# Kernel optimization log

Hardware: AMD Instinct MI355X
Metric: run time of the kernel (lower is better)

The kernel has to match this reference:

```python
import jax, jax.numpy as jnp
import numpy as np

GROUPS = 8   # GroupNorm groups used by create_pat_conv*_blocks(..., groups=8)
EPS = 1e-5
K = 20       # num_neighbor


def group_norm(x, gamma, beta):
    # x: [B, C, ...spatial]
    B, C = x.shape[0], x.shape[1]
    shape = x.shape
    xg = x.reshape(B, GROUPS, C // GROUPS, -1)
    m = xg.mean(axis=(2, 3), keepdims=True)
    v = ((xg - m) ** 2).mean(axis=(2, 3), keepdims=True)
    xg = (xg - m) * jax.lax.rsqrt(v + EPS)
    x = xg.reshape(shape)
    bshape = (1, C) + (1,) * (len(shape) - 2)
    return x * gamma.reshape(bshape) + beta.reshape(bshape)


def conv_block(x, w, b, gamma, beta):
    # pointwise (kernel-size 1) conv + GroupNorm + ELU, works for 1d and 2d spatial
    y = jnp.einsum('oc,bc...->bo...', w, x) + b.reshape((1, -1) + (1,) * (x.ndim - 2))
    return jax.nn.elu(group_norm(y, gamma, beta))


def knn_graph(points, k):
    # points: [B, 3, N] -> neighbor coords [B, 3, N, k] (self included, dilation=1)
    sq = jnp.sum(points * points, axis=1)                      # [B, N]
    inner = jnp.einsum('bci,bcj->bij', points, points)         # [B, N, N]
    dist = sq[:, :, None] + sq[:, None, :] - 2.0 * inner       # squared pairwise dist
    _, idx = jax.lax.top_k(-dist, k)                           # [B, N, k] smallest dists
    neighbors = jnp.take_along_axis(points[:, :, None, :], idx[:, None, :, :], axis=3)
    return neighbors                                           # [B, 3, N, k]


def setup_inputs() -> dict:
    key = jax.random.key(0)
    B, N = 4, 8192
    dims1 = [6, 32, 64]
    dims2 = [64, 512, 1024]
    keys = iter(jax.random.split(key, 32))
    inp = {"points": jax.random.normal(next(keys), (B, 3, N), dtype=jnp.float32)}
    for tag, dims in (("p1", dims1), ("p2", dims2)):
        for i in range(len(dims) - 1):
            cin, cout = dims[i], dims[i + 1]
            inp[f"{tag}_w{i}"] = jax.random.normal(next(keys), (cout, cin), dtype=jnp.float32) / np.float32(np.sqrt(cin))
            inp[f"{tag}_b{i}"] = jnp.zeros((cout,), dtype=jnp.float32)
            inp[f"{tag}_g{i}"] = jnp.ones((cout,), dtype=jnp.float32)
            inp[f"{tag}_beta{i}"] = jnp.zeros((cout,), dtype=jnp.float32)
    return inp


def reference(points, p1_w0, p1_b0, p1_g0, p1_beta0, p1_w1, p1_b1, p1_g1, p1_beta1,
              p2_w0, p2_b0, p2_g0, p2_beta0, p2_w1, p2_b1, p2_g1, p2_beta1):
    neighbors = knn_graph(points, K)                             # [B, 3, N, K]
    center = jnp.broadcast_to(points[:, :, :, None], neighbors.shape)
    x = jnp.concatenate([center, neighbors - center], axis=1)   # [B, 6, N, K]
    x = conv_block(x, p1_w0, p1_b0, p1_g0, p1_beta0)            # [B, 32, N, K]
    x = conv_block(x, p1_w1, p1_b1, p1_g1, p1_beta1)            # [B, 64, N, K]
    x = jnp.max(x, axis=2)                                      # [B, 64, K] (faithful to source: max over dim=2)
    x = conv_block(x, p2_w0, p2_b0, p2_g0, p2_beta0)            # [B, 512, K]
    x = conv_block(x, p2_w1, p2_b1, p2_g1, p2_beta1)            # [B, 1024, K]
    return x
```

## Files before the change

kernel.cpp:

```cpp
#include <hip/hip_runtime.h>
#include <math.h>

#define NPTS   8192
#define BATCH  4
#define KNN    20
#define NKTOT  (NPTS*KNN)
#define EPS    1e-5f
#define FQC    64

#define WINW   3072
#define WITR   (WINW/4/128)
#define GWIN   2048
#define GITR   (GWIN/4/128)
#define NBIN   1024
#define BIN_LO (-4.5f)
#define BIN_W  (9.0f/1024.0f)

typedef float v2f __attribute__((ext_vector_type(2)));

__device__ __forceinline__ float elu(float x) { return x > 0.0f ? x : expm1f(x); }
__device__ __forceinline__ float eluf(float x) { return x > 0.0f ? x : __expf(x) - 1.0f; }
__device__ __forceinline__ v2f splat2(float x) { v2f v; v.x = x; v.y = x; return v; }
__device__ __forceinline__ float rfl(float x) {
    return __uint_as_float(__builtin_amdgcn_readfirstlane(__float_as_uint(x)));
}

__device__ __forceinline__ unsigned fenc(float f) {
    unsigned b = __float_as_uint(f);
    return b ^ ((unsigned)(((int)b) >> 31) | 0x80000000u);
}
__device__ __forceinline__ float fdec(unsigned u) {
    unsigned b = (u & 0x80000000u) ? (u ^ 0x80000000u) : ~u;
    return __uint_as_float(b);
}

__device__ __forceinline__ int xbin(float x) {
    int bin = (int)floorf((x + 4.5f) * (1024.0f / 9.0f));
    return bin < 0 ? 0 : (bin > NBIN - 1 ? NBIN - 1 : bin);
}

__device__ __forceinline__ unsigned long long packkey(float s, int orig, int slot) {
    return ((unsigned long long)fenc(s) << 32)
         | (unsigned)(((NPTS - 1 - orig) << 13) | slot);
}

__global__ __launch_bounds__(256) void prep_kernel(const float* __restrict__ points,
                                                   float4* __restrict__ pts4,
                                                   float* __restrict__ zeroreg,
                                                   unsigned* __restrict__ minenc,
                                                   unsigned* __restrict__ fcnt,
                                                   int* __restrict__ Pcur_part)
{
    __shared__ int lh[NBIN];
    const int t = blockIdx.x * 256 + threadIdx.x;
    const int b = t >> 13, n = t & (NPTS - 1);
    for (int i = threadIdx.x; i < NBIN; i += 256) lh[i] = 0;
    const float* px = points + b * 3 * NPTS;
    float x = px[n], y = px[NPTS + n], z = px[2 * NPTS + n];
    pts4[t] = make_float4(x, y, z, -0.5f * (x * x + y * y + z * z));
    if (t < 18176) zeroreg[t] = 0.f;
    if (t < 5120)  minenc[t] = 0xFFFFFFFFu;
    if (t < 8)     fcnt[t] = 0u;
    __syncthreads();
    atomicAdd(&lh[xbin(x)], 1);
    __syncthreads();
    for (int i = threadIdx.x; i < NBIN; i += 256)
        Pcur_part[blockIdx.x * NBIN + i] = lh[i];
}

__global__ __launch_bounds__(256) void scatter_kernel(const float4* __restrict__ pts4,
                                                      const int* __restrict__ Pcur_part,
                                                      float4* __restrict__ psort,
                                                      int* __restrict__ sidx,
                                                      int* __restrict__ binof)
{
    __shared__ int boff[NBIN];
    __shared__ int brank[NBIN];
    __shared__ int wsum[256];
    const int jb = blockIdx.x & 31;
    const int b  = blockIdx.x >> 5;
    const int tt = threadIdx.x;
    const int t0 = tt * 4;

    int tot0 = 0, tot1 = 0, tot2 = 0, tot3 = 0;
    int pre0 = 0, pre1 = 0, pre2 = 0, pre3 = 0;
    for (int p = 0; p < 32; ++p) {
        const int4 c = *(const int4*)&Pcur_part[(b * 32 + p) * NBIN + t0];
        tot0 += c.x; tot1 += c.y; tot2 += c.z; tot3 += c.w;
        if (p < jb) { pre0 += c.x; pre1 += c.y; pre2 += c.z; pre3 += c.w; }
    }
    const int tsum = tot0 + tot1 + tot2 + tot3;
    wsum[tt] = tsum;
    __syncthreads();
    for (int off = 1; off < 256; off <<= 1) {
        int a = (tt >= off) ? wsum[tt - off] : 0;
        __syncthreads();
        wsum[tt] += a;
        __syncthreads();
    }
    int run = wsum[tt] - tsum;
    boff[t0 + 0] = run + pre0; run += tot0;
    boff[t0 + 1] = run + pre1; run += tot1;
    boff[t0 + 2] = run + pre2; run += tot2;
    boff[t0 + 3] = run + pre3;
    for (int i = tt; i < NBIN; i += 256) brank[i] = 0;
    __syncthreads();

    const int n = jb * 256 + tt;
    float4 p = pts4[b * NPTS + n];
    int bin = xbin(p.x);
    int slot = boff[bin] + atomicAdd(&brank[bin], 1);
    psort[b * NPTS + slot] = p;
    sidx [b * NPTS + slot] = n;
    binof[b * NPTS + slot] = bin;
}

__global__ __launch_bounds__(256, 8) void knn_win_kernel(
    const float4* __restrict__ psort, const int* __restrict__ sidx,
    const int* __restrict__ binof, int* __restrict__ idx_out,
    unsigned* __restrict__ fcnt, int* __restrict__ flist)
{
    __shared__ unsigned long long queue[8][FQC];
    __shared__ float smaxs[4][8][64];
    __shared__ float gates[8];
    __shared__ int qcnt[8];

    const int tid  = threadIdx.x;
    const int lane = tid & 63;
    const int wv   = tid >> 6;
    const int b    = blockIdx.x >> 10;
    const int oct  = blockIdx.x & 1023;
    const int q0s  = oct * 8;
    const float4* psb = psort + b * NPTS;
    const int*    six = sidx  + b * NPTS;
    const int*    bob = binof + b * NPTS;

    int s = q0s + 4 - WINW / 2;
    if (s < 0) s = 0;
    if (s > NPTS - WINW) s = NPTS - WINW;
    int gs = q0s + 4 - GWIN / 2;
    if (gs < 0) gs = 0;
    if (gs > NPTS - GWIN) gs = NPTS - GWIN;

    if (tid < 8) qcnt[tid] = 0;

    float qx[8], qy[8], qz[8], q2[8];
    v2f smax2[8];
#pragma unroll
    for (int q = 0; q < 8; ++q) {
        float4 qp = psb[q0s + q];
        qx[q] = rfl(qp.x); qy[q] = rfl(qp.y); qz[q] = rfl(qp.z);
        q2[q] = rfl(-(qp.w + qp.w));
        smax2[q] = splat2(-INFINITY);
    }

    const int gbase = gs + (((lane >> 5) * 4 + wv) << 6) + ((lane & 31) << 1);
    const int lbase = s  + (((lane >> 5) * 4 + wv) << 6) + ((lane & 31) << 1);

#pragma unroll
    for (int t = 0; t < GITR; ++t) {
        float4 p0 = psb[gbase + t * 512];
        float4 p1 = psb[gbase + t * 512 + 1];
        v2f px = { p0.x, p1.x }, py = { p0.y, p1.y };
        v2f pz = { p0.z, p1.z }, pw = { p0.w, p1.w };
#pragma unroll
        for (int q = 0; q < 8; ++q) {
            v2f sv = __builtin_elementwise_fma(splat2(qx[q]), px,
                     __builtin_elementwise_fma(splat2(qy[q]), py,
                     __builtin_elementwise_fma(splat2(qz[q]), pz, pw)));
            smax2[q] = __builtin_elementwise_max(smax2[q], sv);
        }
    }
#pragma unroll
    for (int q = 0; q < 8; ++q) smaxs[wv][q][lane] = fmaxf(smax2[q].x, smax2[q].y);
    __syncthreads();

#pragma unroll
    for (int qq = 0; qq < 2; ++qq) {
        const int q = wv * 2 + qq;
        float v = fmaxf(fmaxf(smaxs[0][q][lane], smaxs[1][q][lane]),
                        fmaxf(smaxs[2][q][lane], smaxs[3][q][lane]));
#pragma unroll
        for (int k = 2; k <= 64; k <<= 1)
#pragma unroll
            for (int j = k >> 1; j >= 1; j >>= 1) {
                float o = __shfl_xor(v, j);
                bool up = ((lane & k) == 0);
                bool keepmin = (((lane & j) == 0) == up);
                v = keepmin ? fminf(v, o) : fmaxf(v, o);
            }
        float m = __shfl(v, 44);
        if (lane == 0) gates[q] = m - 1e-4f - 1e-5f * fabsf(m);
    }
    __syncthreads();
    float sgate[8];
#pragma unroll
    for (int q = 0; q < 8; ++q) sgate[q] = gates[q];

#pragma unroll
    for (int t = 0; t < WITR; ++t) {
        const int jb = lbase + t * 512;
        float4 p0 = psb[jb];
        float4 p1 = psb[jb + 1];
        v2f px = { p0.x, p1.x }, py = { p0.y, p1.y };
        v2f pz = { p0.z, p1.z }, pw = { p0.w, p1.w };
#pragma unroll
        for (int q = 0; q < 8; ++q) {
            v2f sv = __builtin_elementwise_fma(splat2(qx[q]), px,
                     __builtin_elementwise_fma(splat2(qy[q]), py,
                     __builtin_elementwise_fma(splat2(qz[q]), pz, pw)));
            if (fmaxf(sv.x, sv.y) >= sgate[q]) {
#pragma unroll
                for (int h = 0; h < 2; ++h) {
                    float svh = h ? sv.y : sv.x;
                    if (svh >= sgate[q]) {
                        int slot = atomicAdd(&qcnt[q], 1);
                        if (slot < FQC)
                            queue[q][slot] = packkey(svh, six[jb + h], jb + h);
                    }
                }
            }
        }
    }
    __syncthreads();

    float xLe = (s == 0) ? -3.0e38f
                         : (BIN_LO + (float)(bob[s] + 1) * BIN_W);
    float xRe = (s == NPTS - WINW) ? 3.0e38f
                         : (BIN_LO + (float)bob[s + WINW] * BIN_W);

#pragma unroll
    for (int qq = 0; qq < 2; ++qq) {
        const int q = wv * 2 + qq;
        const int cr = qcnt[q];
        const bool ovf = (cr > FQC);
        const int c = cr < FQC ? cr : FQC;
        unsigned long long key = (lane < c) ? queue[q][lane] : 0ull;
#pragma unroll
        for (int k = 2; k <= 64; k <<= 1)
#pragma unroll
            for (int j = k >> 1; j >= 1; j >>= 1) {
                unsigned long long o = __shfl_xor(key, j);
                bool up = ((lane & k) == 0);
                bool keepmax = (((lane & j) == 0) == up);
                bool omax = o > key;
                key = (keepmax == omax) ? o : key;
            }
        if (lane < KNN)
            idx_out[(b * KNN + lane) * NPTS + (q0s + q)] =
                (int)(unsigned)(key & 0x1FFFu);

        unsigned long long k19 = __shfl(key, 19);
        float s20 = fdec((unsigned)(k19 >> 32));
        float d20 = fmaxf(q2[q] - 2.0f * s20, 0.0f);
        float mg  = 1e-3f + 1e-3f * d20;
        float dL  = qx[q] - xLe;
        float dR  = xRe - qx[q];
        bool ok = !ovf && (c >= KNN) && dL > 0.0f && dR > 0.0f
                  && (d20 + mg < dL * dL) && (d20 + mg < dR * dR);
        if (!ok && lane == 0) {
            unsigned fs = atomicAdd(&fcnt[b], 1u);
            if (fs < 8192u) flist[b * 8192 + fs] = q0s + q;
        }
    }
}

__global__ __launch_bounds__(256, 8) void knn_fb_kernel(const float4* __restrict__ psort,
                                                        const int* __restrict__ sidx,
                                                        int* __restrict__ idx_out,
                                                        const unsigned* __restrict__ fcnt,
                                                        const int* __restrict__ flist)
{
    __shared__ unsigned long long queue[2][FQC];
    __shared__ float smaxs[4][2][64];
    __shared__ float gates[2];
    __shared__ int qcnt[2];

    const int tid  = threadIdx.x;
    const int lane = tid & 63;
    const int wv   = tid >> 6;
    const int bb   = blockIdx.x & 3;
    unsigned cnt = fcnt[bb];
    if (cnt > 8192u) cnt = 8192u;
    if (cnt == 0u) return;
    const float4* pb = psort + bb * NPTS;
    const int* six = sidx + bb * NPTS;
    const int* fl = flist + bb * 8192;
    const int cbase = wv * (NPTS / 4);
    const int tstep = gridDim.x >> 2;

    for (int task = blockIdx.x >> 2; task * 2 < (int)cnt; task += tstep) {
        int qs[2];
        float qx[2], qy[2], qz[2];
        v2f smax2[2];
        if (tid < 2) qcnt[tid] = 0;
#pragma unroll
        for (int q = 0; q < 2; ++q) {
            int e = task * 2 + q;
            if (e >= (int)cnt) e = (int)cnt - 1;
            qs[q] = __builtin_amdgcn_readfirstlane(fl[e]);
            float4 qp = pb[qs[q]];
            qx[q] = rfl(qp.x); qy[q] = rfl(qp.y); qz[q] = rfl(qp.z);
            smax2[q] = splat2(-INFINITY);
        }

#pragma unroll 4
        for (int t = 0; t < NPTS / 4 / 128; ++t) {
            float4 p0 = pb[cbase + t * 128 + 2 * lane];
            float4 p1 = pb[cbase + t * 128 + 2 * lane + 1];
            v2f px = { p0.x, p1.x }, py = { p0.y, p1.y };
            v2f pz = { p0.z, p1.z }, pw = { p0.w, p1.w };
#pragma unroll
            for (int q = 0; q < 2; ++q) {
                v2f sv = __builtin_elementwise_fma(splat2(qx[q]), px,
                         __builtin_elementwise_fma(splat2(qy[q]), py,
                         __builtin_elementwise_fma(splat2(qz[q]), pz, pw)));
                smax2[q] = __builtin_elementwise_max(smax2[q], sv);
            }
        }
#pragma unroll
        for (int q = 0; q < 2; ++q) smaxs[wv][q][lane] = fmaxf(smax2[q].x, smax2[q].y);
        __syncthreads();

        if (wv < 2) {
            const int q = wv;
            float v = fmaxf(fmaxf(smaxs[0][q][lane], smaxs[1][q][lane]),
                            fmaxf(smaxs[2][q][lane], smaxs[3][q][lane]));
#pragma unroll
            for (int k = 2; k <= 64; k <<= 1)
#pragma unroll
                for (int j = k >> 1; j >= 1; j >>= 1) {
                    float o = __shfl_xor(v, j);
                    bool up = ((lane & k) == 0);
                    bool keepmin = (((lane & j) == 0) == up);
                    v = keepmin ? fminf(v, o) : fmaxf(v, o);
                }
            float m = __shfl(v, 44);
            if (lane == 0) gates[q] = m - 1e-4f - 1e-5f * fabsf(m);
        }
        __syncthreads();
        float sg0 = gates[0], sg1 = gates[1];

        for (int t = 0; t < NPTS / 4 / 128; ++t) {
            const int jb = cbase + t * 128 + 2 * lane;
            float4 p0 = pb[jb];
            float4 p1 = pb[jb + 1];
            v2f px = { p0.x, p1.x }, py = { p0.y, p1.y };
            v2f pz = { p0.z, p1.z }, pw = { p0.w, p1.w };
#pragma unroll
            for (int q = 0; q < 2; ++q) {
                float sg = q ? sg1 : sg0;
                v2f sv = __builtin_elementwise_fma(splat2(qx[q]), px,
                         __builtin_elementwise_fma(splat2(qy[q]), py,
                         __builtin_elementwise_fma(splat2(qz[q]), pz, pw)));
                if (fmaxf(sv.x, sv.y) >= sg) {
#pragma unroll
                    for (int h = 0; h < 2; ++h) {
                        float svh = h ? sv.y : sv.x;
                        if (svh >= sg) {
                            int slot = atomicAdd(&qcnt[q], 1);
                            if (slot < FQC)
                                queue[q][slot] = packkey(svh, six[jb + h], jb + h);
                        }
                    }
                }
            }
        }
        __syncthreads();

        if (wv < 2) {
            const int q = wv;
            int c = qcnt[q]; c = c < FQC ? c : FQC;
            unsigned long long key = (lane < c) ? queue[q][lane] : 0ull;
#pragma unroll
            for (int k = 2; k <= 64; k <<= 1)
#pragma unroll
                for (int j = k >> 1; j >= 1; j >>= 1) {
                    unsigned long long o = __shfl_xor(key, j);
                    bool up = ((lane & k) == 0);
                    bool keepmax = (((lane & j) == 0) == up);
                    bool omax = o > key;
                    key = (keepmax == omax) ? o : key;
                }
            if (lane < KNN)
                idx_out[(bb * KNN + lane) * NPTS + qs[q]] =
                    (int)(unsigned)(key & 0x1FFFu);
        }
        __syncthreads();
    }
}

__global__ __launch_bounds__(256) void moments_x_kernel(const float4* __restrict__ psort,
                                                        const int* __restrict__ idx,
                                                        float* __restrict__ sums1p)
{
    const int b  = blockIdx.x / 80;
    const int r0 = (blockIdx.x - b * 80) * 2048;
    const float4* pb = psort + b * NPTS;
    const int* ib = idx + b * NKTOT;

    float v[27];
#pragma unroll
    for (int i = 0; i < 27; ++i) v[i] = 0.f;

    for (int e = 0; e < 8; ++e) {
        const int id = r0 + e * 256 + threadIdx.x;
        const int n = id & (NPTS - 1);
        const int j = ib[id];
        float4 c4 = pb[n];
        float4 e4 = pb[j];
        float x[6] = { c4.x, c4.y, c4.z, e4.x - c4.x, e4.y - c4.y, e4.z - c4.z };
        int p = 6;
#pragma unroll
        for (int d = 0; d < 6; ++d) {
            v[d] += x[d];
#pragma unroll
            for (int ee = d; ee < 6; ++ee) v[p++] += x[d] * x[ee];
        }
    }
#pragma unroll
    for (int i = 0; i < 27; ++i)
        for (int o = 32; o > 0; o >>= 1) v[i] += __shfl_xor(v[i], o);

    __shared__ float red[4][27];
    const int lane = threadIdx.x & 63, w = threadIdx.x >> 6;
    if (lane == 0)
#pragma unroll
        for (int i = 0; i < 27; ++i) red[w][i] = v[i];
    __syncthreads();
    if (threadIdx.x < 27) {
        float acc = red[0][threadIdx.x] + red[1][threadIdx.x] + red[2][threadIdx.x] + red[3][threadIdx.x];
        int slot = blockIdx.x & 63;
        atomicAdd(&sums1p[(slot * BATCH + b) * 27 + threadIdx.x], acc);
    }
}

__global__ void finalize1_kernel(const float* __restrict__ sums1p,
                                 const float* __restrict__ w1, const float* __restrict__ b1,
                                 const float* __restrict__ g1, const float* __restrict__ beta1,
                                 float* __restrict__ w1f)
{
    __shared__ float S[BATCH][27];
    const int t = threadIdx.x;
    if (t < 108) {
        int b = t / 27, i = t % 27;
        float acc = 0.f;
        for (int s = 0; s < 64; ++s) acc += sums1p[(s * BATCH + b) * 27 + i];
        S[b][i] = acc;
    }
    __syncthreads();
    const int b = t >> 5, c = t & 31;
    const float invS = 1.0f / (float)NKTOT;
    float Ex[6], M[6][6];
#pragma unroll
    for (int d = 0; d < 6; ++d) Ex[d] = S[b][d] * invS;
    int p = 6;
#pragma unroll
    for (int d = 0; d < 6; ++d)
#pragma unroll
        for (int e = d; e < 6; ++e) { float v = S[b][p++] * invS; M[d][e] = v; M[e][d] = v; }
    const int g = c >> 2;
    float msum = 0.f, qsum = 0.f;
    for (int cc = g * 4; cc < g * 4 + 4; ++cc) {
        float w[6];
#pragma unroll
        for (int d = 0; d < 6; ++d) w[d] = w1[cc * 6 + d];
        float dotEx = 0.f;
#pragma unroll
        for (int d = 0; d < 6; ++d) dotEx += w[d] * Ex[d];
        float Ey = dotEx + b1[cc];
        float Ey2 = 0.f;
#pragma unroll
        for (int d = 0; d < 6; ++d)
#pragma unroll
            for (int e = 0; e < 6; ++e) Ey2 += w[d] * w[e] * M[d][e];
        Ey2 += 2.0f * b1[cc] * dotEx + b1[cc] * b1[cc];
        msum += Ey; qsum += Ey2;
    }
    float m = msum * 0.25f;
    float var = qsum * 0.25f - m * m;
    float inv = rsqrtf(var + EPS);
    float s = g1[c] * inv;
    float tt = s * (b1[c] - m) + beta1[c];
    float* o = w1f + (b * 32 + c) * 8;
#pragma unroll
    for (int d = 0; d < 6; ++d) o[d] = s * w1[c * 6 + d];
    o[6] = tt; o[7] = 0.f;
}

__global__ __launch_bounds__(256, 3) void fused_main_kernel(
    const float4* __restrict__ psort, const int* __restrict__ idxb,
    const float* __restrict__ w1f, const float* __restrict__ w2, const float* __restrict__ b2,
    float* __restrict__ sums2p, unsigned int* __restrict__ maxenc, unsigned int* __restrict__ minenc)
{
    __shared__ __align__(16) float w2t[32 * 64];
    __shared__ __align__(16) float z1s[32 * 256];
    __shared__ __align__(16) float4 w1s4[64];
    __shared__ float b2s[64];
    __shared__ float redmx[256], redmn[256], sqred[64];

    const int t   = threadIdx.x;
    const int blk = blockIdx.x;
    const int nc  = blk & 15;
    const int k   = (blk >> 4) % 20;
    const int b   = blk / 320;

    for (int i = t; i < 512; i += 256) {
        float4 v = ((const float4*)w2)[i];
        int c = i >> 3, kq = (i & 7) * 4;
        w2t[(kq + 0) * 64 + c] = v.x; w2t[(kq + 1) * 64 + c] = v.y;
        w2t[(kq + 2) * 64 + c] = v.z; w2t[(kq + 3) * 64 + c] = v.w;
    }
    if (t < 64) { w1s4[t] = ((const float4*)w1f)[b * 64 + t]; b2s[t] = b2[t]; }

    const int wvi = t >> 6;
    const int cg8 = t & 7;
    const int n0  = (t >> 3) * 8;
    const int c0  = cg8 * 8;
    const float4* pb = psort + b * NPTS;
    const int nbase = nc * 512;
    const int* idxrow = idxb + (b * KNN + k) * NPTS;

    float mx[8], mn[8];
#pragma unroll
    for (int ci = 0; ci < 8; ++ci) { mx[ci] = -INFINITY; mn[ci] = INFINITY; }
    float gs = 0.f, gq = 0.f;

    for (int ph = 0; ph < 2; ++ph) {
        const int n = nbase + ph * 256 + t;
        const int j = idxrow[n];
        float4 c4 = pb[n];
        float4 e4 = pb[j];
        float x0[6] = { c4.x, c4.y, c4.z, e4.x - c4.x, e4.y - c4.y, e4.z - c4.z };

        __syncthreads();
#pragma unroll
        for (int c = 0; c < 32; ++c) {
            float4 wA = w1s4[c * 2 + 0];
            float4 wB = w1s4[c * 2 + 1];
            float z = wB.z;
            z = fmaf(wA.x, x0[0], z); z = fmaf(wA.y, x0[1], z); z = fmaf(wA.z, x0[2], z);
            z = fmaf(wA.w, x0[3], z); z = fmaf(wB.x, x0[4], z); z = fmaf(wB.y, x0[5], z);
            z1s[c * 256 + t] = eluf(z);
        }
        __syncthreads();

        float acc[8][8];
#pragma unroll
        for (int ci = 0; ci < 8; ++ci) {
            float bb = b2s[c0 + ci];
#pragma unroll
            for (int pj = 0; pj < 8; ++pj) acc[ci][pj] = bb;
        }
#pragma unroll
        for (int kk = 0; kk < 32; ++kk) {
            float4 a0 = *(const float4*)&w2t[kk * 64 + c0];
            float4 a1 = *(const float4*)&w2t[kk * 64 + c0 + 4];
            float4 z0 = *(const float4*)&z1s[kk * 256 + n0];
            float4 z1v = *(const float4*)&z1s[kk * 256 + n0 + 4];
            float avv[8] = { a0.x, a0.y, a0.z, a0.w, a1.x, a1.y, a1.z, a1.w };
            float zvv[8] = { z0.x, z0.y, z0.z, z0.w, z1v.x, z1v.y, z1v.z, z1v.w };
#pragma unroll
            for (int ci = 0; ci < 8; ++ci)
#pragma unroll
                for (int pj = 0; pj < 8; ++pj) acc[ci][pj] = fmaf(avv[ci], zvv[pj], acc[ci][pj]);
        }
#pragma unroll
        for (int ci = 0; ci < 8; ++ci)
#pragma unroll
            for (int pj = 0; pj < 8; ++pj) {
                float v = acc[ci][pj];
                gs += v; gq = fmaf(v, v, gq);
                mx[ci] = fmaxf(mx[ci], v); mn[ci] = fminf(mn[ci], v);
            }
    }

#pragma unroll
    for (int m = 8; m <= 32; m <<= 1) {
#pragma unroll
        for (int ci = 0; ci < 8; ++ci) {
            mx[ci] = fmaxf(mx[ci], __shfl_xor(mx[ci], m));
            mn[ci] = fminf(mn[ci], __shfl_xor(mn[ci], m));
        }
        gs += __shfl_xor(gs, m);
        gq += __shfl_xor(gq, m);
    }
    if ((t & 63) < 8) {
        const int l = t & 7;
#pragma unroll
        for (int ci = 0; ci < 8; ++ci) {
            redmx[wvi * 64 + l * 8 + ci] = mx[ci];
            redmn[wvi * 64 + l * 8 + ci] = mn[ci];
        }
        sqred[(wvi * 8 + l) * 2 + 0] = gs;
        sqred[(wvi * 8 + l) * 2 + 1] = gq;
    }
    __syncthreads();
    if (t < 64) {
        float m = fmaxf(fmaxf(redmx[t], redmx[64 + t]), fmaxf(redmx[128 + t], redmx[192 + t]));
        atomicMax(&maxenc[(b * 64 + t) * KNN + k], fenc(m));
    } else if (t < 128) {
        int c = t - 64;
        float m = fminf(fminf(redmn[c], redmn[64 + c]), fminf(redmn[128 + c], redmn[192 + c]));
        atomicMin(&minenc[(b * 64 + c) * KNN + k], fenc(m));
    } else if (t < 144) {
        int i2 = t - 128, g = i2 >> 1, w = i2 & 1;
        float v = 0.f;
#pragma unroll
        for (int wv2 = 0; wv2 < 4; ++wv2)
            v += sqred[(wv2 * 8 + g) * 2 + w];
        int slot = blk & 63;
        atomicAdd(&sums2p[((slot * BATCH + b) * 8 + g) * 2 + w], v);
    }
}

__global__ void build_m1_kernel(const float* __restrict__ sums2p,
                                const unsigned int* __restrict__ maxenc,
                                const unsigned int* __restrict__ minenc,
                                const float* __restrict__ gamma, const float* __restrict__ beta,
                                float* __restrict__ m1)
{
    const int t = blockIdx.x * 256 + threadIdx.x;
    const int b = t / 1280;
    const int r = t - b * 1280;
    const int c = r / 20;
    const int g = c >> 3;
    float s = 0.f, q = 0.f;
    for (int sl = 0; sl < 64; ++sl) {
        s += sums2p[((sl * BATCH + b) * 8 + g) * 2 + 0];
        q += sums2p[((sl * BATCH + b) * 8 + g) * 2 + 1];
    }
    const float cnt = 8.0f * (float)NKTOT;
    float m = s / cnt;
    float var = q / cnt - m * m;
    float inv = rsqrtf(var + EPS);
    float sc = gamma[c] * inv;
    float tt = beta[c] - sc * m;
    float y = (sc >= 0.f) ? fdec(maxenc[t]) : fdec(minenc[t]);
    m1[t] = elu(sc * y + tt);
}

template <int CIN, int SLOTS>
__global__ void p2_gemm_kernel(const float* __restrict__ zin, const float* __restrict__ w,
                               const float* __restrict__ bias, float* __restrict__ yout,
                               float* __restrict__ sumsp, int chans_per_group)
{
    const int t = blockIdx.x * 256 + threadIdx.x;
    const int per_b = (gridDim.x * 256) / BATCH;
    const int b = t / per_b;
    const int r = t - b * per_b;
    const int o = r / 20;
    const int k = r - o * 20;
    const float* zb = zin + b * CIN * 20;
    const float* wrow = w + o * CIN;
    float acc = bias[o];
    for (int c = 0; c < CIN; c += 4) {
        float4 wv = *(const float4*)&wrow[c];
        acc += wv.x * zb[(c + 0) * 20 + k] + wv.y * zb[(c + 1) * 20 + k]
             + wv.z * zb[(c + 2) * 20 + k] + wv.w * zb[(c + 3) * 20 + k];
    }
    yout[t] = acc;

    __shared__ float ls[16];
    if (threadIdx.x < 16) ls[threadIdx.x] = 0.f;
    __syncthreads();
    const int g = o / chans_per_group;
    atomicAdd(&ls[g * 2 + 0], acc);
    atomicAdd(&ls[g * 2 + 1], acc * acc);
    __syncthreads();
    if (threadIdx.x < 16) {
        int slot = blockIdx.x & (SLOTS - 1);
        atomicAdd(&sumsp[(slot * BATCH + b) * 16 + threadIdx.x], ls[threadIdx.x]);
    }
}

template <int SLOTS>
__global__ void p2_finalize_kernel(const float* __restrict__ y, const float* __restrict__ sumsp,
                                   const float* __restrict__ gamma, const float* __restrict__ beta,
                                   float* __restrict__ z, int chans_per_group, float cnt)
{
    const int t = blockIdx.x * 256 + threadIdx.x;
    const int per_b = (gridDim.x * 256) / BATCH;
    const int b = t / per_b;
    const int r = t - b * per_b;
    const int o = r / 20;
    const int g = o / chans_per_group;
    float s = 0.f, q = 0.f;
    for (int sl = 0; sl < SLOTS; ++sl) {
        s += sumsp[(sl * BATCH + b) * 16 + g * 2 + 0];
        q += sumsp[(sl * BATCH + b) * 16 + g * 2 + 1];
    }
    float m = s / cnt;
    float var = q / cnt - m * m;
    float inv = rsqrtf(var + EPS);
    float v = gamma[o] * inv * (y[t] - m) + beta[o];
    z[t] = elu(v);
}

extern "C" void kernel_launch(void* const* d_in, const int* in_sizes, int n_in,
                              void* d_out, int out_size, void* d_ws, size_t ws_size,
                              hipStream_t stream)
{
    const float* points  = (const float*)d_in[0];
    const float* p1_w0   = (const float*)d_in[1];
    const float* p1_b0   = (const float*)d_in[2];
    const float* p1_g0   = (const float*)d_in[3];
    const float* p1_bt0  = (const float*)d_in[4];
    const float* p1_w1   = (const float*)d_in[5];
    const float* p1_b1   = (const float*)d_in[6];
    const float* p1_g1   = (const float*)d_in[7];
    const float* p1_bt1  = (const float*)d_in[8];
    const float* p2_w0   = (const float*)d_in[9];
    const float* p2_b0   = (const float*)d_in[10];
    const float* p2_g0   = (const float*)d_in[11];
    const float* p2_bt0  = (const float*)d_in[12];
    const float* p2_w1   = (const float*)d_in[13];
    const float* p2_b1   = (const float*)d_in[14];
    const float* p2_g1   = (const float*)d_in[15];
    const float* p2_bt1  = (const float*)d_in[16];
    float* out = (float*)d_out;

    float* ws = (float*)d_ws;
    int*      idx     = (int*)ws;
    float*    sums1p  = ws + 655360;
    float*    sums2p  = sums1p + 6912;
    float*    sumsAp  = sums2p + 4096;
    float*    sumsBp  = sumsAp + 1024;
    unsigned* maxenc  = (unsigned*)(sumsBp + 1024);
    unsigned* minenc  = maxenc + 5120;
    float*    w1f     = (float*)(minenc + 5120);
    float*    m1      = w1f + 1024;
    float*    yp2a    = m1 + 5120;
    float*    zp2a    = yp2a + 40960;
    float*    yp2b    = zp2a + 40960;
    float4*   pts4    = (float4*)yp2a;
    int*      Pcur_part = idx;
    float*    psortf  = yp2b + 81920;
    float4*   psort4  = (float4*)psortf;
    int*      sidx    = (int*)(psortf + 131072);
    int*      binof   = sidx + 32768;
    unsigned* fcnt8   = (unsigned*)(binof + 32768 + 64);
    int*      flist   = (int*)(fcnt8 + 64);

    prep_kernel<<<128, 256, 0, stream>>>(points, pts4, sums1p, minenc, fcnt8, Pcur_part);
    scatter_kernel<<<128, 256, 0, stream>>>(pts4, Pcur_part, psort4, sidx, binof);
    knn_win_kernel<<<4096, 256, 0, stream>>>(psort4, sidx, binof, idx, fcnt8, flist);
    knn_fb_kernel<<<4096, 256, 0, stream>>>(psort4, sidx, idx, fcnt8, flist);
    moments_x_kernel<<<320, 256, 0, stream>>>(psort4, idx, sums1p);
    finalize1_kernel<<<1, 128, 0, stream>>>(sums1p, p1_w0, p1_b0, p1_g0, p1_bt0, w1f);
    fused_main_kernel<<<1280, 256, 0, stream>>>(psort4, idx, w1f, p1_w1, p1_b1,
                                                sums2p, maxenc, minenc);
    build_m1_kernel<<<20, 256, 0, stream>>>(sums2p, maxenc, minenc, p1_g1, p1_bt1, m1);
    p2_gemm_kernel<64, 16><<<160, 256, 0, stream>>>(m1, p2_w0, p2_b0, yp2a, sumsAp, 64);
    p2_finalize_kernel<16><<<160, 256, 0, stream>>>(yp2a, sumsAp, p2_g0, p2_bt0, zp2a, 64, 1280.0f);
    p2_gemm_kernel<512, 16><<<320, 256, 0, stream>>>(zp2a, p2_w1, p2_b1, yp2b, sumsBp, 128);
    p2_finalize_kernel<16><<<320, 256, 0, stream>>>(yp2b, sumsBp, p2_g1, p2_bt1, out, 128, 2560.0f);
}
```

Measured before the change: 266.4 us.

## Restrict KNN fallback scan to x-bin range bounded by current 20th neighbor

The fallback KNN kernel used to scan all 8192 sorted points for each pair of failed queries. It now handles one query per task. It reads the window pass's current 20th neighbor to get a radius, then binary-searches the x-sorted bin array to find the slice of points that can lie within that radius, and runs both the max-gate pass and the candidate pass only over that slice. This removes most of the full-array scans, but gives up the two-queries-per-block amortization and adds a serial binary search plus extra barriers per query. Correctness depends on the window pass's 20th neighbor being a valid upper bound, including for queries that overflowed.

```diff
diff --git a/kernel.cpp b/kernel.cpp
--- a/kernel.cpp
+++ b/kernel.cpp
@@ -267,14 +267,15 @@
 
 __global__ __launch_bounds__(256, 8) void knn_fb_kernel(const float4* __restrict__ psort,
                                                         const int* __restrict__ sidx,
+                                                        const int* __restrict__ binof,
                                                         int* __restrict__ idx_out,
                                                         const unsigned* __restrict__ fcnt,
                                                         const int* __restrict__ flist)
 {
-    __shared__ unsigned long long queue[2][FQC];
-    __shared__ float smaxs[4][2][64];
-    __shared__ float gates[2];
-    __shared__ int qcnt[2];
+    __shared__ unsigned long long queue[FQC];
+    __shared__ float smaxs[4][64];
+    __shared__ float sh_gate;
+    __shared__ int sh_lo, sh_hi, qcnt;
 
     const int tid  = threadIdx.x;
     const int lane = tid & 63;
@@ -285,47 +286,52 @@
     if (cnt == 0u) return;
     const float4* pb = psort + bb * NPTS;
     const int* six = sidx + bb * NPTS;
+    const int* bob = binof + bb * NPTS;
     const int* fl = flist + bb * 8192;
-    const int cbase = wv * (NPTS / 4);
     const int tstep = gridDim.x >> 2;
 
-    for (int task = blockIdx.x >> 2; task * 2 < (int)cnt; task += tstep) {
-        int qs[2];
-        float qx[2], qy[2], qz[2];
-        v2f smax2[2];
-        if (tid < 2) qcnt[tid] = 0;
-#pragma unroll
-        for (int q = 0; q < 2; ++q) {
-            int e = task * 2 + q;
-            if (e >= (int)cnt) e = (int)cnt - 1;
-            qs[q] = __builtin_amdgcn_readfirstlane(fl[e]);
-            float4 qp = pb[qs[q]];
-            qx[q] = rfl(qp.x); qy[q] = rfl(qp.y); qz[q] = rfl(qp.z);
-            smax2[q] = splat2(-INFINITY);
-        }
-
-#pragma unroll 4
-        for (int t = 0; t < NPTS / 4 / 128; ++t) {
-            float4 p0 = pb[cbase + t * 128 + 2 * lane];
-            float4 p1 = pb[cbase + t * 128 + 2 * lane + 1];
-            v2f px = { p0.x, p1.x }, py = { p0.y, p1.y };
-            v2f pz = { p0.z, p1.z }, pw = { p0.w, p1.w };
-#pragma unroll
-            for (int q = 0; q < 2; ++q) {
-                v2f sv = __builtin_elementwise_fma(splat2(qx[q]), px,
-                         __builtin_elementwise_fma(splat2(qy[q]), py,
-                         __builtin_elementwise_fma(splat2(qz[q]), pz, pw)));
-                smax2[q] = __builtin_elementwise_max(smax2[q], sv);
-            }
-        }
-#pragma unroll
-        for (int q = 0; q < 2; ++q) smaxs[wv][q][lane] = fmaxf(smax2[q].x, smax2[q].y);
-        __syncthreads();
-
-        if (wv < 2) {
-            const int q = wv;
-            float v = fmaxf(fmaxf(smaxs[0][q][lane], smaxs[1][q][lane]),
-                            fmaxf(smaxs[2][q][lane], smaxs[3][q][lane]));
+    for (int task = blockIdx.x >> 2; task < (int)cnt; task += tstep) {
+        const int qs = __builtin_amdgcn_readfirstlane(fl[task]);
+        float4 qp = pb[qs];
+        const float qx = rfl(qp.x), qy = rfl(qp.y), qz = rfl(qp.z);
+        const float q2 = rfl(-(qp.w + qp.w));
+
+        const int s19 = __builtin_amdgcn_readfirstlane(
+                            idx_out[(bb * KNN + 19) * NPTS + qs]);
+        float4 p19 = pb[s19];
+        float s20 = fmaf(qx, p19.x, fmaf(qy, p19.y, fmaf(qz, p19.z, p19.w)));
+        float R2 = fmaxf(q2 - 2.0f * s20, 0.0f) * 1.002f + 1e-3f;
+        float R = sqrtf(R2);
+        const int lo_bin = xbin(qx - R), hi_bin = xbin(qx + R);
+
+        if (tid < 2) {
+            const int T = (tid == 0) ? lo_bin : hi_bin + 1;
+            int l = 0, r = NPTS;
+            while (l < r) { int m = (l + r) >> 1; if (bob[m] >= T) r = m; else l = m + 1; }
+            if (tid == 0) { sh_lo = l; qcnt = 0; } else sh_hi = l;
+        }
+        __syncthreads();
+        const int lo = sh_lo, hi = sh_hi;
+        const int iters = (hi - lo + 511) >> 9;
+
+        v2f smax2 = splat2(-INFINITY);
+        for (int t = 0; t < iters; ++t) {
+            const int p0i = lo + t * 512 + wv * 128 + 2 * lane;
+            float4 a = (p0i     < hi) ? pb[p0i]     : make_float4(0.f, 0.f, 0.f, -3.0e38f);
+            float4 c = (p0i + 1 < hi) ? pb[p0i + 1] : make_float4(0.f, 0.f, 0.f, -3.0e38f);
+            v2f px = { a.x, c.x }, py = { a.y, c.y };
+            v2f pz = { a.z, c.z }, pw = { a.w, c.w };
+            v2f sv = __builtin_elementwise_fma(splat2(qx), px,
+                     __builtin_elementwise_fma(splat2(qy), py,
+                     __builtin_elementwise_fma(splat2(qz), pz, pw)));
+            smax2 = __builtin_elementwise_max(smax2, sv);
+        }
+        smaxs[wv][lane] = fmaxf(smax2.x, smax2.y);
+        __syncthreads();
+
+        if (wv == 0) {
+            float v = fmaxf(fmaxf(smaxs[0][lane], smaxs[1][lane]),
+                            fmaxf(smaxs[2][lane], smaxs[3][lane]));
 #pragma unroll
             for (int k = 2; k <= 64; k <<= 1)
 #pragma unroll
@@ -336,42 +342,37 @@
                     v = keepmin ? fminf(v, o) : fmaxf(v, o);
                 }
             float m = __shfl(v, 44);
-            if (lane == 0) gates[q] = m - 1e-4f - 1e-5f * fabsf(m);
-        }
-        __syncthreads();
-        float sg0 = gates[0], sg1 = gates[1];
-
-        for (int t = 0; t < NPTS / 4 / 128; ++t) {
-            const int jb = cbase + t * 128 + 2 * lane;
-            float4 p0 = pb[jb];
-            float4 p1 = pb[jb + 1];
-            v2f px = { p0.x, p1.x }, py = { p0.y, p1.y };
-            v2f pz = { p0.z, p1.z }, pw = { p0.w, p1.w };
-#pragma unroll
-            for (int q = 0; q < 2; ++q) {
-                float sg = q ? sg1 : sg0;
-                v2f sv = __builtin_elementwise_fma(splat2(qx[q]), px,
-                         __builtin_elementwise_fma(splat2(qy[q]), py,
-                         __builtin_elementwise_fma(splat2(qz[q]), pz, pw)));
-                if (fmaxf(sv.x, sv.y) >= sg) {
-#pragma unroll
-                    for (int h = 0; h < 2; ++h) {
-                        float svh = h ? sv.y : sv.x;
-                        if (svh >= sg) {
-                            int slot = atomicAdd(&qcnt[q], 1);
-                            if (slot < FQC)
-                                queue[q][slot] = packkey(svh, six[jb + h], jb + h);
-                        }
+            if (lane == 0) sh_gate = m - 1e-4f - 1e-5f * fabsf(m);
+        }
+        __syncthreads();
+        const float gate = sh_gate;
+
+        for (int t = 0; t < iters; ++t) {
+            const int p0i = lo + t * 512 + wv * 128 + 2 * lane;
+            float4 a = (p0i     < hi) ? pb[p0i]     : make_float4(0.f, 0.f, 0.f, -3.0e38f);
+            float4 c = (p0i + 1 < hi) ? pb[p0i + 1] : make_float4(0.f, 0.f, 0.f, -3.0e38f);
+            v2f px = { a.x, c.x }, py = { a.y, c.y };
+            v2f pz = { a.z, c.z }, pw = { a.w, c.w };
+            v2f sv = __builtin_elementwise_fma(splat2(qx), px,
+                     __builtin_elementwise_fma(splat2(qy), py,
+                     __builtin_elementwise_fma(splat2(qz), pz, pw)));
+            if (fmaxf(sv.x, sv.y) >= gate) {
+#pragma unroll
+                for (int h = 0; h < 2; ++h) {
+                    float svh = h ? sv.y : sv.x;
+                    if (svh >= gate) {
+                        int slot = atomicAdd(&qcnt, 1);
+                        if (slot < FQC)
+                            queue[slot] = packkey(svh, six[p0i + h], p0i + h);
                     }
                 }
             }
         }
         __syncthreads();
 
-        if (wv < 2) {
-            const int q = wv;
-            int c = qcnt[q]; c = c < FQC ? c : FQC;
-            unsigned long long key = (lane < c) ? queue[q][lane] : 0ull;
+        if (wv == 0) {
+            int c = qcnt; c = c < FQC ? c : FQC;
+            unsigned long long key = (lane < c) ? queue[lane] : 0ull;
 #pragma unroll
             for (int k = 2; k <= 64; k <<= 1)
 #pragma unroll
@@ -383,7 +384,7 @@
                     key = (keepmax == omax) ? o : key;
                 }
             if (lane < KNN)
-                idx_out[(bb * KNN + lane) * NPTS + qs[q]] =
+                idx_out[(bb * KNN + lane) * NPTS + qs] =
                     (int)(unsigned)(key & 0x1FFFu);
         }
         __syncthreads();
@@ -745,7 +746,7 @@
     prep_kernel<<<128, 256, 0, stream>>>(points, pts4, sums1p, minenc, fcnt8, Pcur_part);
     scatter_kernel<<<128, 256, 0, stream>>>(pts4, Pcur_part, psort4, sidx, binof);
     knn_win_kernel<<<4096, 256, 0, stream>>>(psort4, sidx, binof, idx, fcnt8, flist);
-    knn_fb_kernel<<<4096, 256, 0, stream>>>(psort4, sidx, idx, fcnt8, flist);
+    knn_fb_kernel<<<4096, 256, 0, stream>>>(psort4, sidx, binof, idx, fcnt8, flist);
     moments_x_kernel<<<320, 256, 0, stream>>>(psort4, idx, sums1p);
     finalize1_kernel<<<1, 128, 0, stream>>>(sums1p, p1_w0, p1_b0, p1_g0, p1_bt0, w1f);
     fused_main_kernel<<<1280, 256, 0, stream>>>(psort4, idx, w1f, p1_w1, p1_b1,
```

New measurement: 267.9 us. About the same (+0.6%).
